# Kernel tuning notes

Hardware: AMD Instinct MI355X
Metric: run time of the kernel (lower is better)

The kernel has to match this reference:

```python
import jax, jax.numpy as jnp
import numpy as np

U_DECAY = 0.97
X_DECAY = 0.97
LN_EPS = 1e-5   # torch F.layer_norm default
L1_EPS = 1e-12  # torch F.normalize default


def _ln(x):
    # layer_norm over last dim, no affine params
    m = jnp.mean(x, axis=-1, keepdims=True)
    v = jnp.mean((x - m) ** 2, axis=-1, keepdims=True)
    return (x - m) * jax.lax.rsqrt(v + LN_EPS)


def setup_inputs() -> dict:
    key = jax.random.key(0)
    k0, k1, k2, k3 = jax.random.split(key, 4)
    B, T, d, n = 8, 256, 256, 1024
    embeddings = jax.random.normal(k0, (B, T, d), dtype=jnp.float32)
    E = jax.random.normal(k1, (d, n), dtype=jnp.float32) / n ** 0.5
    Dx = jax.random.normal(k2, (n, d), dtype=jnp.float32) / d ** 0.5
    Dy = jax.random.normal(k3, (n, d), dtype=jnp.float32) / d ** 0.5
    return {"embeddings": embeddings, "E": E, "Dx": Dx, "Dy": Dy}


def reference(embeddings, E, Dx, Dy):
    B, T, d = embeddings.shape
    n = E.shape[1]

    def step(carry, v_prev):  # v_prev: (B, d)
        x_state, rho = carry  # (B, n), (B, d, n)
        x_update = jax.nn.relu(v_prev @ Dx.T)                      # (B, n)
        x_t = X_DECAY * x_state + x_update
        x_t = x_t / jnp.maximum(jnp.sum(jnp.abs(x_t), axis=-1, keepdims=True), L1_EPS)  # L1 normalize
        a_star = jnp.einsum('bdn,bn->bd', rho, x_t)                # (B, d)
        y_core = _ln(a_star) @ Dy.T                                # (B, n)
        y_t = jax.nn.relu(y_core) * jax.nn.relu(x_t)               # (B, n)
        v_star = _ln(y_t @ E.T)                                    # (B, d)
        rho_t = U_DECAY * rho + _ln(v_prev)[:, :, None] * x_t[:, None, :]  # (B, d, n)
        return (x_t, rho_t), v_star

    x0 = jnp.zeros((B, n), dtype=embeddings.dtype)
    rho0 = jnp.zeros((B, d, n), dtype=embeddings.dtype)
    _, vs = jax.lax.scan(step, (x0, rho0), jnp.swapaxes(embeddings, 0, 1))  # vs: (T, B, d)
    return jnp.swapaxes(vs, 0, 1)  # (B, T, d)
```

## Files before the change

### kernel.cpp

```cpp
#include <hip/hip_runtime.h>
#include <math.h>


#define TT 256
#define BB 8
#define DD 256
#define NN 1024
#define ROWS (BB*TT)

using f16   = _Float16;
using f16x4 = __attribute__((ext_vector_type(4))) _Float16;
using f16x8 = __attribute__((ext_vector_type(8))) _Float16;
using f32x4 = __attribute__((ext_vector_type(4))) float;

__device__ inline f32x4 mfma16(f16x8 a, f16x8 b, f32x4 c) {
    return __builtin_amdgcn_mfma_f32_16x16x32_f16(a, b, c, 0, 0, 0);
}

__launch_bounds__(256)
__global__ void cvtln_kernel(const float* __restrict__ emb, const float* __restrict__ E,
                             const float* __restrict__ Dx, const float* __restrict__ Dy,
                             f16* __restrict__ embf, f16* __restrict__ Ef,
                             f16* __restrict__ Dxf, f16* __restrict__ Dyf,
                             f16* __restrict__ lnvTf) {
    __shared__ f16 sT[256][24];
    if (blockIdx.x < 1280) {
        int base = (blockIdx.x * 256 + threadIdx.x) * 4;
        const float* s; f16* d; int loc;
        if      (base <  524288) { s = emb; d = embf; loc = base; }
        else if (base <  786432) { s = E;   d = Ef;   loc = base - 524288; }
        else if (base < 1048576) { s = Dx;  d = Dxf;  loc = base - 786432; }
        else                     { s = Dy;  d = Dyf;  loc = base - 1048576; }
        float4 v = *(const float4*)(s + loc);
        f16x4 h = {(f16)v.x, (f16)v.y, (f16)v.z, (f16)v.w};
        *(f16x4*)(d + loc) = h;
        return;
    }
    const int bx = blockIdx.x - 1280;
    const int b  = bx >> 4;
    const int t0 = (bx & 15) * 16;
    const int wave = threadIdx.x >> 6;
    const int lane = threadIdx.x & 63;
#pragma unroll
    for (int rr = 0; rr < 4; ++rr) {
        int tloc = wave * 4 + rr;
        const float* p = emb + ((size_t)b * TT + t0 + tloc) * DD;
        float4 v = *(const float4*)(p + lane * 4);
        float s  = v.x + v.y + v.z + v.w;
        float s2 = v.x*v.x + v.y*v.y + v.z*v.z + v.w*v.w;
#pragma unroll
        for (int o = 32; o; o >>= 1) {
            s  += __shfl_xor(s,  o, 64);
            s2 += __shfl_xor(s2, o, 64);
        }
        float m   = s * (1.0f / 256.0f);
        float sc  = rsqrtf(s2 * (1.0f / 256.0f) - m * m + 1e-5f);
        sT[lane * 4 + 0][tloc] = (f16)((v.x - m) * sc);
        sT[lane * 4 + 1][tloc] = (f16)((v.y - m) * sc);
        sT[lane * 4 + 2][tloc] = (f16)((v.z - m) * sc);
        sT[lane * 4 + 3][tloc] = (f16)((v.w - m) * sc);
    }
    __syncthreads();
    int j = threadIdx.x;
    size_t o = ((size_t)b * DD + j) * TT + t0;
    *(f16x8*)(lnvTf + o)     = *(const f16x8*)&sT[j][0];
    *(f16x8*)(lnvTf + o + 8) = *(const f16x8*)&sT[j][8];
}

__launch_bounds__(256)
__global__ void k_xu(const f16* __restrict__ A, const f16* __restrict__ B,
                     f16* __restrict__ xuh, float* __restrict__ Spart) {
    const int i0 = blockIdx.y * 64, j0 = blockIdx.x * 128;
    const int t = threadIdx.x, lane = t & 63, wid = t >> 6;
    const int wr = wid >> 1, wc = wid & 1;
    const int lr = lane >> 4, lc = lane & 15;
    __shared__ __align__(16) f16 sA[2][64][40], sB[2][128][40];
    __shared__ float ssum[64][2];
    const int arow = t >> 2, akq = (t & 3) * 8;
    f32x4 acc[2][4];
    const f32x4 z4 = {0.f, 0.f, 0.f, 0.f};
#pragma unroll
    for (int fi = 0; fi < 2; ++fi)
#pragma unroll
        for (int fj = 0; fj < 4; ++fj) acc[fi][fj] = z4;

    const int NT = DD / 32;
    const f16* pa  = A + (size_t)(i0 + arow) * DD + akq;
    const f16* pb0 = B + (size_t)(j0 + arow) * DD + akq;
    const f16* pb1 = B + (size_t)(j0 + 64 + arow) * DD + akq;
    f16x8 va  = *(const f16x8*)pa;
    f16x8 vb0 = *(const f16x8*)pb0;
    f16x8 vb1 = *(const f16x8*)pb1;
    *(f16x8*)&sA[0][arow][akq]      = va;
    *(f16x8*)&sB[0][arow][akq]      = vb0;
    *(f16x8*)&sB[0][64 + arow][akq] = vb1;
    __syncthreads();
    int cur = 0;
    for (int kt = 0; kt < NT; ++kt) {
        if (kt + 1 < NT) {
            int ko = (kt + 1) * 32;
            va  = *(const f16x8*)(pa + ko);
            vb0 = *(const f16x8*)(pb0 + ko);
            vb1 = *(const f16x8*)(pb1 + ko);
        }
        f16x8 ah[2], bh[4];
#pragma unroll
        for (int fi = 0; fi < 2; ++fi)
            ah[fi] = *(const f16x8*)&sA[cur][wr * 32 + fi * 16 + lc][lr * 8];
#pragma unroll
        for (int fj = 0; fj < 4; ++fj)
            bh[fj] = *(const f16x8*)&sB[cur][wc * 64 + fj * 16 + lc][lr * 8];
#pragma unroll
        for (int fi = 0; fi < 2; ++fi)
#pragma unroll
            for (int fj = 0; fj < 4; ++fj)
                acc[fi][fj] = mfma16(ah[fi], bh[fj], acc[fi][fj]);
        if (kt + 1 < NT) {
            *(f16x8*)&sA[cur ^ 1][arow][akq]      = va;
            *(f16x8*)&sB[cur ^ 1][arow][akq]      = vb0;
            *(f16x8*)&sB[cur ^ 1][64 + arow][akq] = vb1;
            __syncthreads();
            cur ^= 1;
        }
    }
    float rs[2][4] = {};
#pragma unroll
    for (int fi = 0; fi < 2; ++fi)
#pragma unroll
        for (int fj = 0; fj < 4; ++fj) {
            f32x4 d = acc[fi][fj];
#pragma unroll
            for (int r = 0; r < 4; ++r) {
                int i = i0 + wr * 32 + fi * 16 + lr * 4 + r;
                int j = j0 + wc * 64 + fj * 16 + lc;
                float vv = fmaxf(d[r], 0.f);
                xuh[(size_t)i * NN + j] = (f16)vv;
                rs[fi][r] += vv;
            }
        }
#pragma unroll
    for (int fi = 0; fi < 2; ++fi)
#pragma unroll
        for (int r = 0; r < 4; ++r) {
            float v = rs[fi][r];
#pragma unroll
            for (int m = 1; m < 16; m <<= 1) v += __shfl_xor(v, m, 64);
            if (lc == 0) ssum[wr * 32 + fi * 16 + lr * 4 + r][wc] = v;
        }
    __syncthreads();
    if (t < 64) Spart[(size_t)blockIdx.x * ROWS + i0 + t] = ssum[t][0] + ssum[t][1];
}

__launch_bounds__(256)
__global__ void k_xscan(const f16* __restrict__ xuh, const float* __restrict__ Spart,
                        f16* __restrict__ xf) {
    __shared__ float Gs[16][16], Hs[16][16], Cs[16][16];
    __shared__ float sS[256], sRC[256];
    __shared__ int bad;
    const int b = blockIdx.x >> 6, jgrp = blockIdx.x & 63;
    const int tid = threadIdx.x;
    float s = 0.f;
#pragma unroll
    for (int g = 0; g < 8; ++g) s += Spart[(size_t)g * ROWS + b * TT + tid];
    if (tid == 0) bad = 0;
    sS[tid] = s;
    __syncthreads();
    float us = (tid == 0) ? s : (0.97f + s);
    if (us < 1e-12f) bad = 1;
    __syncthreads();
    if (!bad) {
        sRC[tid] = 1.0f / us;
    } else if (tid == 0) {
        float sigma = 0.f;
        for (int tt = 0; tt < TT; ++tt) {
            float u2 = fmaf(0.97f, sigma, sS[tt]);
            float r  = 1.0f / fmaxf(u2, 1e-12f);
            sRC[tt] = r;
            sigma = u2 * r;
        }
    }
    __syncthreads();

    const int ck = tid >> 4, jl = tid & 15;
    const int j  = jgrp * 16 + jl;
    const size_t base = ((size_t)b * TT + ck * 16) * NN + j;
    float xur[16], rcr[16];
#pragma unroll
    for (int i = 0; i < 16; ++i) xur[i] = (float)xuh[base + (size_t)i * NN];
#pragma unroll
    for (int i = 0; i < 16; ++i) rcr[i] = sRC[ck * 16 + i];
    float xs = 0.f, G = 1.f;
#pragma unroll
    for (int i = 0; i < 16; ++i) {
        xs = fmaf(0.97f, xs, xur[i]) * rcr[i];
        G *= 0.97f * rcr[i];
    }
    Gs[ck][jl] = G;
    Hs[ck][jl] = xs;
    __syncthreads();
    if (tid < 16) {
        float cr = 0.f;
        Cs[0][tid] = 0.f;
#pragma unroll
        for (int cc = 0; cc < 15; ++cc) {
            cr = fmaf(Gs[cc][tid], cr, Hs[cc][tid]);
            Cs[cc + 1][tid] = cr;
        }
    }
    __syncthreads();
    xs = Cs[ck][jl];
#pragma unroll
    for (int i = 0; i < 16; ++i) {
        xs = fmaf(0.97f, xs, xur[i]) * rcr[i];
        xf[base + (size_t)i * NN] = (f16)xs;
    }
}

template <int EPI>
__launch_bounds__(256)
__global__ void g64_kernel(const f16* __restrict__ A, const f16* __restrict__ B,
                           float* __restrict__ Cf, f16* __restrict__ Ch,
                           int N, int ld, int Kloop,
                           long long sA_, long long sB_, long long sC_) {
    const int z = blockIdx.z;
    A += (size_t)z * sA_; B += (size_t)z * sB_;
    if (EPI == 0) Cf += (size_t)z * sC_; else Ch += (size_t)z * sC_;
    const int i0 = blockIdx.y * 64, j0 = blockIdx.x * 64;
    const int t = threadIdx.x, lane = t & 63, wid = t >> 6;
    const int wr = wid >> 1, wc = wid & 1;
    const int lr = lane >> 4, lc = lane & 15;
    const float L2D = -0.043943348f;

    if (EPI == 3 && j0 > i0) {
#pragma unroll
        for (int fi = 0; fi < 2; ++fi)
#pragma unroll
            for (int fj = 0; fj < 2; ++fj)
#pragma unroll
                for (int r = 0; r < 4; ++r) {
                    int i = i0 + wr * 32 + fi * 16 + lr * 4 + r;
                    int j = j0 + wc * 32 + fj * 16 + lc;
                    Ch[(size_t)i * N + j] = (f16)0.f;
                }
        return;
    }

    __shared__ __align__(16) f16 sA[2][64][40], sB[2][64][40];
    const int srow = t >> 2, skq = (t & 3) * 8;
    f32x4 acc[2][2];
    const f32x4 z4 = {0.f, 0.f, 0.f, 0.f};
    acc[0][0] = z4; acc[0][1] = z4; acc[1][0] = z4; acc[1][1] = z4;

    const int NT = Kloop / 32;
    const f16* pa = A + (size_t)(i0 + srow) * ld + skq;
    const f16* pb = B + (size_t)(j0 + srow) * ld + skq;
    f16x8 va = *(const f16x8*)pa;
    f16x8 vb = *(const f16x8*)pb;
    *(f16x8*)&sA[0][srow][skq] = va;
    *(f16x8*)&sB[0][srow][skq] = vb;
    __syncthreads();
    int cur = 0;
    for (int kt = 0; kt < NT; ++kt) {
        if (kt + 1 < NT) {
            va = *(const f16x8*)(pa + (kt + 1) * 32);
            vb = *(const f16x8*)(pb + (kt + 1) * 32);
        }
        f16x8 ah0 = *(const f16x8*)&sA[cur][wr * 32 + lc][lr * 8];
        f16x8 ah1 = *(const f16x8*)&sA[cur][wr * 32 + 16 + lc][lr * 8];
        f16x8 bh0 = *(const f16x8*)&sB[cur][wc * 32 + lc][lr * 8];
        f16x8 bh1 = *(const f16x8*)&sB[cur][wc * 32 + 16 + lc][lr * 8];
        acc[0][0] = mfma16(ah0, bh0, acc[0][0]);
        acc[0][1] = mfma16(ah0, bh1, acc[0][1]);
        acc[1][0] = mfma16(ah1, bh0, acc[1][0]);
        acc[1][1] = mfma16(ah1, bh1, acc[1][1]);
        if (kt + 1 < NT) {
            *(f16x8*)&sA[cur ^ 1][srow][skq] = va;
            *(f16x8*)&sB[cur ^ 1][srow][skq] = vb;
            __syncthreads();
            cur ^= 1;
        }
    }
#pragma unroll
    for (int fi = 0; fi < 2; ++fi)
#pragma unroll
        for (int fj = 0; fj < 2; ++fj) {
            f32x4 d = acc[fi][fj];
#pragma unroll
            for (int r = 0; r < 4; ++r) {
                int i = i0 + wr * 32 + fi * 16 + lr * 4 + r;
                int j = j0 + wc * 32 + fj * 16 + lc;
                size_t o = (size_t)i * N + j;
                if (EPI == 0) {
                    Cf[o] = d[r];
                } else {
                    float w = 0.f;
                    if (j < i) w = exp2f((float)(i - 1 - j) * L2D) * d[r];
                    Ch[o] = (f16)w;
                }
            }
        }
}

__launch_bounds__(256)
__global__ void k_aln(const f16* __restrict__ Wf, const f16* __restrict__ lnvTf,
                      f16* __restrict__ alnf) {
    const int b = blockIdx.y;
    const int i0 = blockIdx.x * 16;
    const f16* A = Wf + (size_t)b * TT * TT;
    const f16* B = lnvTf + (size_t)b * DD * TT;
    const int t = threadIdx.x, lane = t & 63, w = t >> 6;
    const int lr = lane >> 4, lc = lane & 15;
    __shared__ __align__(16) f16 sA[2][16][40], sB[2][256][40];
    __shared__ float sS[4][16], sS2[4][16];
    const int arow = t >> 2, akq = (t & 3) * 8;
    const int brow = t >> 2, bkq = (t & 3) * 8;
    f32x4 acc[4];
    const f32x4 z4 = {0.f, 0.f, 0.f, 0.f};
#pragma unroll
    for (int f = 0; f < 4; ++f) acc[f] = z4;

    const int NT = TT / 32;
    const f16* pa = A + (size_t)(i0 + arow) * TT + akq;
    const f16* pb = B + (size_t)brow * TT + bkq;
    f16x8 va;
    f16x8 vb[4];
    if (t < 64) va = *(const f16x8*)pa;
#pragma unroll
    for (int q = 0; q < 4; ++q)
        vb[q] = *(const f16x8*)(pb + (size_t)q * 64 * TT);
    if (t < 64) *(f16x8*)&sA[0][arow][akq] = va;
#pragma unroll
    for (int q = 0; q < 4; ++q)
        *(f16x8*)&sB[0][q * 64 + brow][bkq] = vb[q];
    __syncthreads();
    int cur = 0;
    for (int kt = 0; kt < NT; ++kt) {
        if (kt + 1 < NT) {
            int ko = (kt + 1) * 32;
            if (t < 64) va = *(const f16x8*)(pa + ko);
#pragma unroll
            for (int q = 0; q < 4; ++q)
                vb[q] = *(const f16x8*)(pb + (size_t)q * 64 * TT + ko);
        }
        f16x8 af = *(const f16x8*)&sA[cur][lc][lr * 8];
#pragma unroll
        for (int f = 0; f < 4; ++f) {
            f16x8 bf = *(const f16x8*)&sB[cur][w * 64 + f * 16 + lc][lr * 8];
            acc[f] = mfma16(af, bf, acc[f]);
        }
        if (kt + 1 < NT) {
            if (t < 64) *(f16x8*)&sA[cur ^ 1][arow][akq] = va;
#pragma unroll
            for (int q = 0; q < 4; ++q)
                *(f16x8*)&sB[cur ^ 1][q * 64 + brow][bkq] = vb[q];
            __syncthreads();
            cur ^= 1;
        }
    }
    float s[4] = {}, s2[4] = {};
#pragma unroll
    for (int f = 0; f < 4; ++f)
#pragma unroll
        for (int r = 0; r < 4; ++r) { float v = acc[f][r]; s[r] += v; s2[r] += v * v; }
#pragma unroll
    for (int m = 1; m < 16; m <<= 1)
#pragma unroll
        for (int r = 0; r < 4; ++r) {
            s[r]  += __shfl_xor(s[r],  m, 64);
            s2[r] += __shfl_xor(s2[r], m, 64);
        }
    if (lc == 0)
#pragma unroll
        for (int r = 0; r < 4; ++r) { sS[w][lr * 4 + r] = s[r]; sS2[w][lr * 4 + r] = s2[r]; }
    __syncthreads();
    float mean[4], rstd[4];
#pragma unroll
    for (int r = 0; r < 4; ++r) {
        int row = lr * 4 + r;
        float tot  = sS[0][row] + sS[1][row] + sS[2][row] + sS[3][row];
        float tot2 = sS2[0][row] + sS2[1][row] + sS2[2][row] + sS2[3][row];
        mean[r] = tot * (1.f / 256.f);
        rstd[r] = rsqrtf(tot2 * (1.f / 256.f) - mean[r] * mean[r] + 1e-5f);
    }
#pragma unroll
    for (int f = 0; f < 4; ++f)
#pragma unroll
        for (int r = 0; r < 4; ++r) {
            int i = i0 + lr * 4 + r;
            int j = w * 64 + f * 16 + lc;
            alnf[((size_t)b * TT + i) * DD + j] = (f16)((acc[f][r] - mean[r]) * rstd[r]);
        }
}

__launch_bounds__(256)
__global__ void k_y(const f16* __restrict__ A, const f16* __restrict__ B,
                    f16* __restrict__ yf, const f16* __restrict__ xf) {
    const int i0 = blockIdx.y * 64, j0 = blockIdx.x * 128;
    const int t = threadIdx.x, lane = t & 63, wid = t >> 6;
    const int wr = wid >> 1, wc = wid & 1;
    const int lr = lane >> 4, lc = lane & 15;
    __shared__ __align__(16) f16 sA[2][64][40], sB[2][128][40];
    const int arow = t >> 2, akq = (t & 3) * 8;
    f32x4 acc[2][4];
    const f32x4 z4 = {0.f, 0.f, 0.f, 0.f};
#pragma unroll
    for (int fi = 0; fi < 2; ++fi)
#pragma unroll
        for (int fj = 0; fj < 4; ++fj) acc[fi][fj] = z4;

    const int NT = DD / 32;
    const f16* pa  = A + (size_t)(i0 + arow) * DD + akq;
    const f16* pb0 = B + (size_t)(j0 + arow) * DD + akq;
    const f16* pb1 = B + (size_t)(j0 + 64 + arow) * DD + akq;
    f16x8 va  = *(const f16x8*)pa;
    f16x8 vb0 = *(const f16x8*)pb0;
    f16x8 vb1 = *(const f16x8*)pb1;
    *(f16x8*)&sA[0][arow][akq]      = va;
    *(f16x8*)&sB[0][arow][akq]      = vb0;
    *(f16x8*)&sB[0][64 + arow][akq] = vb1;
    __syncthreads();
    int cur = 0;
    for (int kt = 0; kt < NT; ++kt) {
        if (kt + 1 < NT) {
            int ko = (kt + 1) * 32;
            va  = *(const f16x8*)(pa + ko);
            vb0 = *(const f16x8*)(pb0 + ko);
            vb1 = *(const f16x8*)(pb1 + ko);
        }
        f16x8 ah[2], bh[4];
#pragma unroll
        for (int fi = 0; fi < 2; ++fi)
            ah[fi] = *(const f16x8*)&sA[cur][wr * 32 + fi * 16 + lc][lr * 8];
#pragma unroll
        for (int fj = 0; fj < 4; ++fj)
            bh[fj] = *(const f16x8*)&sB[cur][wc * 64 + fj * 16 + lc][lr * 8];
#pragma unroll
        for (int fi = 0; fi < 2; ++fi)
#pragma unroll
            for (int fj = 0; fj < 4; ++fj)
                acc[fi][fj] = mfma16(ah[fi], bh[fj], acc[fi][fj]);
        if (kt + 1 < NT) {
            *(f16x8*)&sA[cur ^ 1][arow][akq]      = va;
            *(f16x8*)&sB[cur ^ 1][arow][akq]      = vb0;
            *(f16x8*)&sB[cur ^ 1][64 + arow][akq] = vb1;
            __syncthreads();
            cur ^= 1;
        }
    }
#pragma unroll
    for (int fi = 0; fi < 2; ++fi)
#pragma unroll
        for (int fj = 0; fj < 4; ++fj) {
            f32x4 d = acc[fi][fj];
#pragma unroll
            for (int r = 0; r < 4; ++r) {
                int i = i0 + wr * 32 + fi * 16 + lr * 4 + r;
                int j = j0 + wc * 64 + fj * 16 + lc;
                size_t o = (size_t)i * NN + j;
                float vv = fmaxf(d[r], 0.f) * (float)xf[o];
                yf[o] = (f16)vv;
            }
        }
}

__launch_bounds__(256)
__global__ void ln2_kernel(const float* __restrict__ in, const float* __restrict__ in2,
                           float* __restrict__ outf) {
    int wave = threadIdx.x >> 6;
    int lane = threadIdx.x & 63;
    int row  = blockIdx.x * 4 + wave;
    float4 v = *(const float4*)(in + (size_t)row * DD + lane * 4);
    float4 w = *(const float4*)(in2 + (size_t)row * DD + lane * 4);
    v.x += w.x; v.y += w.y; v.z += w.z; v.w += w.w;
    float s  = v.x + v.y + v.z + v.w;
    float s2 = v.x*v.x + v.y*v.y + v.z*v.z + v.w*v.w;
#pragma unroll
    for (int o = 32; o; o >>= 1) {
        s  += __shfl_xor(s,  o, 64);
        s2 += __shfl_xor(s2, o, 64);
    }
    float m  = s * (1.0f / 256.0f);
    float sc = rsqrtf(s2 * (1.0f / 256.0f) - m * m + 1e-5f);
    float4 o4 = {(v.x - m) * sc, (v.y - m) * sc, (v.z - m) * sc, (v.w - m) * sc};
    *(float4*)(outf + (size_t)row * DD + lane * 4) = o4;
}

extern "C" void kernel_launch(void* const* d_in, const int* in_sizes, int n_in,
                              void* d_out, int out_size, void* d_ws, size_t ws_size,
                              hipStream_t stream) {
    (void)in_sizes; (void)n_in; (void)out_size; (void)ws_size;
    const float* emb = (const float*)d_in[0];
    const float* E   = (const float*)d_in[1];
    const float* Dx  = (const float*)d_in[2];
    const float* Dy  = (const float*)d_in[3];
    float* out = (float*)d_out;

    char* wsb = (char*)d_ws;
    f16*   embf  = (f16*)(wsb + 0);
    f16*   Ef    = (f16*)(wsb + 1048576);
    f16*   Dxf   = (f16*)(wsb + 1572864);
    f16*   Dyf   = (f16*)(wsb + 2097152);
    f16*   lnvTf = (f16*)(wsb + 2621440);
    f16*   xuh   = (f16*)(wsb + 3670016);
    f16*   xf    = (f16*)(wsb + 7864320);
    f16*   Wf    = (f16*)(wsb + 12058624);
    f16*   alnf  = (f16*)(wsb + 13107200);
    f16*   yf    = (f16*)(wsb + 14155776);
    float* vpart = (float*)(wsb + 18350080);
    float* Spart = (float*)(wsb + 22544384);

    cvtln_kernel<<<1280 + ROWS / 16, 256, 0, stream>>>(
        emb, E, Dx, Dy, embf, Ef, Dxf, Dyf, lnvTf);
    k_xu<<<dim3(NN / 128, ROWS / 64), 256, 0, stream>>>(embf, Dxf, xuh, Spart);
    k_xscan<<<BB * (NN / 16), 256, 0, stream>>>(xuh, Spart, xf);
    g64_kernel<3><<<dim3(TT / 64, TT / 64, BB), 256, 0, stream>>>(
        xf, xf, nullptr, Wf, TT, NN, NN,
        (long long)TT * NN, (long long)TT * NN, (long long)TT * TT);
    k_aln<<<dim3(TT / 16, BB), 256, 0, stream>>>(Wf, lnvTf, alnf);
    k_y<<<dim3(NN / 128, ROWS / 64), 256, 0, stream>>>(alnf, Dyf, yf, xf);
    g64_kernel<0><<<dim3(DD / 64, ROWS / 64, 2), 256, 0, stream>>>(
        yf, Ef, vpart, nullptr, DD, NN, 512,
        512LL, 512LL, (long long)ROWS * DD);
    ln2_kernel<<<ROWS / 4, 256, 0, stream>>>(
        vpart, vpart + (size_t)ROWS * DD, out);
}
```

Baseline: 60.67 us.

## Fuse final LayerNorm into split-K GEMM via atomic counter; widen xscan chunks

Removes the separate ln2 launch. The split-K v GEMM's blocks now increment a per-row-tile atomic counter, and the last of the 8 blocks per row tile sums both K halves and applies LayerNorm, writing the output directly. The counter is zeroed in the first kernel. Separately, the x scan now uses 32-step chunks over 32 columns per block, which halves the block count and shortens the serial carry across chunks, at the cost of more registers per thread. The generic GEMM template is also specialised into a dedicated W kernel.

```diff
diff --git a/kernel.cpp b/kernel.cpp
--- a/kernel.cpp
+++ b/kernel.cpp
@@ -22,8 +22,9 @@
                              const float* __restrict__ Dx, const float* __restrict__ Dy,
                              f16* __restrict__ embf, f16* __restrict__ Ef,
                              f16* __restrict__ Dxf, f16* __restrict__ Dyf,
-                             f16* __restrict__ lnvTf) {
+                             f16* __restrict__ lnvTf, int* __restrict__ cnt) {
     __shared__ f16 sT[256][24];
+    if (blockIdx.x == 0 && threadIdx.x < 32) cnt[threadIdx.x] = 0;
     if (blockIdx.x < 1280) {
         int base = (blockIdx.x * 256 + threadIdx.x) * 4;
         const float* s; f16* d; int loc;
@@ -154,10 +155,10 @@
 __launch_bounds__(256)
 __global__ void k_xscan(const f16* __restrict__ xuh, const float* __restrict__ Spart,
                         f16* __restrict__ xf) {
-    __shared__ float Gs[16][16], Hs[16][16], Cs[16][16];
+    __shared__ float Gs[8][33], Hs[8][33], Cs[8][33];
     __shared__ float sS[256], sRC[256];
     __shared__ int bad;
-    const int b = blockIdx.x >> 6, jgrp = blockIdx.x & 63;
+    const int b = blockIdx.x >> 5, jgrp = blockIdx.x & 31;
     const int tid = threadIdx.x;
     float s = 0.f;
 #pragma unroll
@@ -181,28 +182,28 @@
     }
     __syncthreads();
 
-    const int ck = tid >> 4, jl = tid & 15;
-    const int j  = jgrp * 16 + jl;
-    const size_t base = ((size_t)b * TT + ck * 16) * NN + j;
-    float xur[16], rcr[16];
-#pragma unroll
-    for (int i = 0; i < 16; ++i) xur[i] = (float)xuh[base + (size_t)i * NN];
-#pragma unroll
-    for (int i = 0; i < 16; ++i) rcr[i] = sRC[ck * 16 + i];
+    const int ck = tid >> 5, jl = tid & 31;
+    const int j  = jgrp * 32 + jl;
+    const size_t base = ((size_t)b * TT + ck * 32) * NN + j;
+    float xur[32], rcr[32];
+#pragma unroll
+    for (int i = 0; i < 32; ++i) xur[i] = (float)xuh[base + (size_t)i * NN];
+#pragma unroll
+    for (int i = 0; i < 32; ++i) rcr[i] = sRC[ck * 32 + i];
     float xs = 0.f, G = 1.f;
 #pragma unroll
-    for (int i = 0; i < 16; ++i) {
+    for (int i = 0; i < 32; ++i) {
         xs = fmaf(0.97f, xs, xur[i]) * rcr[i];
         G *= 0.97f * rcr[i];
     }
     Gs[ck][jl] = G;
     Hs[ck][jl] = xs;
     __syncthreads();
-    if (tid < 16) {
+    if (tid < 32) {
         float cr = 0.f;
         Cs[0][tid] = 0.f;
 #pragma unroll
-        for (int cc = 0; cc < 15; ++cc) {
+        for (int cc = 0; cc < 7; ++cc) {
             cr = fmaf(Gs[cc][tid], cr, Hs[cc][tid]);
             Cs[cc + 1][tid] = cr;
         }
@@ -210,28 +211,24 @@
     __syncthreads();
     xs = Cs[ck][jl];
 #pragma unroll
-    for (int i = 0; i < 16; ++i) {
+    for (int i = 0; i < 32; ++i) {
         xs = fmaf(0.97f, xs, xur[i]) * rcr[i];
         xf[base + (size_t)i * NN] = (f16)xs;
     }
 }
 
-template <int EPI>
-__launch_bounds__(256)
-__global__ void g64_kernel(const f16* __restrict__ A, const f16* __restrict__ B,
-                           float* __restrict__ Cf, f16* __restrict__ Ch,
-                           int N, int ld, int Kloop,
-                           long long sA_, long long sB_, long long sC_) {
-    const int z = blockIdx.z;
-    A += (size_t)z * sA_; B += (size_t)z * sB_;
-    if (EPI == 0) Cf += (size_t)z * sC_; else Ch += (size_t)z * sC_;
+__launch_bounds__(256)
+__global__ void k_W(const f16* __restrict__ xf, f16* __restrict__ Wf) {
+    const int b = blockIdx.z;
+    const f16* X = xf + (size_t)b * TT * NN;
+    f16* Wb = Wf + (size_t)b * TT * TT;
     const int i0 = blockIdx.y * 64, j0 = blockIdx.x * 64;
     const int t = threadIdx.x, lane = t & 63, wid = t >> 6;
     const int wr = wid >> 1, wc = wid & 1;
     const int lr = lane >> 4, lc = lane & 15;
     const float L2D = -0.043943348f;
 
-    if (EPI == 3 && j0 > i0) {
+    if (j0 > i0) {
 #pragma unroll
         for (int fi = 0; fi < 2; ++fi)
 #pragma unroll
@@ -240,7 +237,7 @@
                 for (int r = 0; r < 4; ++r) {
                     int i = i0 + wr * 32 + fi * 16 + lr * 4 + r;
                     int j = j0 + wc * 32 + fj * 16 + lc;
-                    Ch[(size_t)i * N + j] = (f16)0.f;
+                    Wb[(size_t)i * TT + j] = (f16)0.f;
                 }
         return;
     }
@@ -251,9 +248,9 @@
     const f32x4 z4 = {0.f, 0.f, 0.f, 0.f};
     acc[0][0] = z4; acc[0][1] = z4; acc[1][0] = z4; acc[1][1] = z4;
 
-    const int NT = Kloop / 32;
-    const f16* pa = A + (size_t)(i0 + srow) * ld + skq;
-    const f16* pb = B + (size_t)(j0 + srow) * ld + skq;
+    const int NT = NN / 32;
+    const f16* pa = X + (size_t)(i0 + srow) * NN + skq;
+    const f16* pb = X + (size_t)(j0 + srow) * NN + skq;
     f16x8 va = *(const f16x8*)pa;
     f16x8 vb = *(const f16x8*)pb;
     *(f16x8*)&sA[0][srow][skq] = va;
@@ -289,14 +286,9 @@
             for (int r = 0; r < 4; ++r) {
                 int i = i0 + wr * 32 + fi * 16 + lr * 4 + r;
                 int j = j0 + wc * 32 + fj * 16 + lc;
-                size_t o = (size_t)i * N + j;
-                if (EPI == 0) {
-                    Cf[o] = d[r];
-                } else {
-                    float w = 0.f;
-                    if (j < i) w = exp2f((float)(i - 1 - j) * L2D) * d[r];
-                    Ch[o] = (f16)w;
-                }
+                float w = 0.f;
+                if (j < i) w = exp2f((float)(i - 1 - j) * L2D) * d[r];
+                Wb[(size_t)i * TT + j] = (f16)w;
             }
         }
 }
@@ -313,7 +305,6 @@
     __shared__ __align__(16) f16 sA[2][16][40], sB[2][256][40];
     __shared__ float sS[4][16], sS2[4][16];
     const int arow = t >> 2, akq = (t & 3) * 8;
-    const int brow = t >> 2, bkq = (t & 3) * 8;
     f32x4 acc[4];
     const f32x4 z4 = {0.f, 0.f, 0.f, 0.f};
 #pragma unroll
@@ -321,7 +312,7 @@
 
     const int NT = TT / 32;
     const f16* pa = A + (size_t)(i0 + arow) * TT + akq;
-    const f16* pb = B + (size_t)brow * TT + bkq;
+    const f16* pb = B + (size_t)arow * TT + akq;
     f16x8 va;
     f16x8 vb[4];
     if (t < 64) va = *(const f16x8*)pa;
@@ -331,7 +322,7 @@
     if (t < 64) *(f16x8*)&sA[0][arow][akq] = va;
 #pragma unroll
     for (int q = 0; q < 4; ++q)
-        *(f16x8*)&sB[0][q * 64 + brow][bkq] = vb[q];
+        *(f16x8*)&sB[0][q * 64 + arow][akq] = vb[q];
     __syncthreads();
     int cur = 0;
     for (int kt = 0; kt < NT; ++kt) {
@@ -352,7 +343,7 @@
             if (t < 64) *(f16x8*)&sA[cur ^ 1][arow][akq] = va;
 #pragma unroll
             for (int q = 0; q < 4; ++q)
-                *(f16x8*)&sB[cur ^ 1][q * 64 + brow][bkq] = vb[q];
+                *(f16x8*)&sB[cur ^ 1][q * 64 + arow][akq] = vb[q];
             __syncthreads();
             cur ^= 1;
         }
@@ -464,25 +455,90 @@
 }
 
 __launch_bounds__(256)
-__global__ void ln2_kernel(const float* __restrict__ in, const float* __restrict__ in2,
-                           float* __restrict__ outf) {
-    int wave = threadIdx.x >> 6;
-    int lane = threadIdx.x & 63;
-    int row  = blockIdx.x * 4 + wave;
-    float4 v = *(const float4*)(in + (size_t)row * DD + lane * 4);
-    float4 w = *(const float4*)(in2 + (size_t)row * DD + lane * 4);
-    v.x += w.x; v.y += w.y; v.z += w.z; v.w += w.w;
-    float s  = v.x + v.y + v.z + v.w;
-    float s2 = v.x*v.x + v.y*v.y + v.z*v.z + v.w*v.w;
-#pragma unroll
-    for (int o = 32; o; o >>= 1) {
-        s  += __shfl_xor(s,  o, 64);
-        s2 += __shfl_xor(s2, o, 64);
-    }
-    float m  = s * (1.0f / 256.0f);
-    float sc = rsqrtf(s2 * (1.0f / 256.0f) - m * m + 1e-5f);
-    float4 o4 = {(v.x - m) * sc, (v.y - m) * sc, (v.z - m) * sc, (v.w - m) * sc};
-    *(float4*)(outf + (size_t)row * DD + lane * 4) = o4;
+__global__ void k_vg(const f16* __restrict__ yf, const f16* __restrict__ Ef,
+                     float* __restrict__ vpart, int* __restrict__ cnt,
+                     float* __restrict__ out) {
+    const int z = blockIdx.z;
+    float* C = vpart + (size_t)z * ROWS * DD;
+    const int i0 = blockIdx.y * 64, j0 = blockIdx.x * 64;
+    const int t = threadIdx.x, lane = t & 63, wid = t >> 6;
+    const int wr = wid >> 1, wc = wid & 1;
+    const int lr = lane >> 4, lc = lane & 15;
+    __shared__ __align__(16) f16 sA[2][64][40], sB[2][64][40];
+    __shared__ int lastFlag;
+    const int srow = t >> 2, skq = (t & 3) * 8;
+    f32x4 acc[2][2];
+    const f32x4 z4 = {0.f, 0.f, 0.f, 0.f};
+    acc[0][0] = z4; acc[0][1] = z4; acc[1][0] = z4; acc[1][1] = z4;
+
+    const int NT = 512 / 32;
+    const f16* pa = yf + (size_t)(i0 + srow) * NN + z * 512 + skq;
+    const f16* pb = Ef + (size_t)(j0 + srow) * NN + z * 512 + skq;
+    f16x8 va = *(const f16x8*)pa;
+    f16x8 vb = *(const f16x8*)pb;
+    *(f16x8*)&sA[0][srow][skq] = va;
+    *(f16x8*)&sB[0][srow][skq] = vb;
+    __syncthreads();
+    int cur = 0;
+    for (int kt = 0; kt < NT; ++kt) {
+        if (kt + 1 < NT) {
+            va = *(const f16x8*)(pa + (kt + 1) * 32);
+            vb = *(const f16x8*)(pb + (kt + 1) * 32);
+        }
+        f16x8 ah0 = *(const f16x8*)&sA[cur][wr * 32 + lc][lr * 8];
+        f16x8 ah1 = *(const f16x8*)&sA[cur][wr * 32 + 16 + lc][lr * 8];
+        f16x8 bh0 = *(const f16x8*)&sB[cur][wc * 32 + lc][lr * 8];
+        f16x8 bh1 = *(const f16x8*)&sB[cur][wc * 32 + 16 + lc][lr * 8];
+        acc[0][0] = mfma16(ah0, bh0, acc[0][0]);
+        acc[0][1] = mfma16(ah0, bh1, acc[0][1]);
+        acc[1][0] = mfma16(ah1, bh0, acc[1][0]);
+        acc[1][1] = mfma16(ah1, bh1, acc[1][1]);
+        if (kt + 1 < NT) {
+            *(f16x8*)&sA[cur ^ 1][srow][skq] = va;
+            *(f16x8*)&sB[cur ^ 1][srow][skq] = vb;
+            __syncthreads();
+            cur ^= 1;
+        }
+    }
+#pragma unroll
+    for (int fi = 0; fi < 2; ++fi)
+#pragma unroll
+        for (int fj = 0; fj < 2; ++fj) {
+            f32x4 d = acc[fi][fj];
+#pragma unroll
+            for (int r = 0; r < 4; ++r) {
+                int i = i0 + wr * 32 + fi * 16 + lr * 4 + r;
+                int j = j0 + wc * 32 + fj * 16 + lc;
+                C[(size_t)i * DD + j] = d[r];
+            }
+        }
+
+    __threadfence();
+    if (t == 0) {
+        int old = atomicAdd(&cnt[blockIdx.y], 1);
+        lastFlag = (old == 7);
+    }
+    __syncthreads();
+    if (!lastFlag) return;
+    __threadfence();
+#pragma unroll
+    for (int u = 0; u < 16; ++u) {
+        int row = i0 + u * 4 + wid;
+        float4 v = *(const float4*)(vpart + (size_t)row * DD + lane * 4);
+        float4 w = *(const float4*)(vpart + (size_t)(ROWS + row) * DD + lane * 4);
+        v.x += w.x; v.y += w.y; v.z += w.z; v.w += w.w;
+        float s  = v.x + v.y + v.z + v.w;
+        float s2 = v.x*v.x + v.y*v.y + v.z*v.z + v.w*v.w;
+#pragma unroll
+        for (int o = 32; o; o >>= 1) {
+            s  += __shfl_xor(s,  o, 64);
+            s2 += __shfl_xor(s2, o, 64);
+        }
+        float m  = s * (1.0f / 256.0f);
+        float sc = rsqrtf(s2 * (1.0f / 256.0f) - m * m + 1e-5f);
+        float4 o4 = {(v.x - m) * sc, (v.y - m) * sc, (v.z - m) * sc, (v.w - m) * sc};
+        *(float4*)(out + (size_t)row * DD + lane * 4) = o4;
+    }
 }
 
 extern "C" void kernel_launch(void* const* d_in, const int* in_sizes, int n_in,
@@ -508,19 +564,14 @@
     f16*   yf    = (f16*)(wsb + 14155776);
     float* vpart = (float*)(wsb + 18350080);
     float* Spart = (float*)(wsb + 22544384);
+    int*   cnt   = (int*)(wsb + 22609920);
 
     cvtln_kernel<<<1280 + ROWS / 16, 256, 0, stream>>>(
-        emb, E, Dx, Dy, embf, Ef, Dxf, Dyf, lnvTf);
+        emb, E, Dx, Dy, embf, Ef, Dxf, Dyf, lnvTf, cnt);
     k_xu<<<dim3(NN / 128, ROWS / 64), 256, 0, stream>>>(embf, Dxf, xuh, Spart);
-    k_xscan<<<BB * (NN / 16), 256, 0, stream>>>(xuh, Spart, xf);
-    g64_kernel<3><<<dim3(TT / 64, TT / 64, BB), 256, 0, stream>>>(
-        xf, xf, nullptr, Wf, TT, NN, NN,
-        (long long)TT * NN, (long long)TT * NN, (long long)TT * TT);
+    k_xscan<<<BB * 32, 256, 0, stream>>>(xuh, Spart, xf);
+    k_W<<<dim3(TT / 64, TT / 64, BB), 256, 0, stream>>>(xf, Wf);
     k_aln<<<dim3(TT / 16, BB), 256, 0, stream>>>(Wf, lnvTf, alnf);
     k_y<<<dim3(NN / 128, ROWS / 64), 256, 0, stream>>>(alnf, Dyf, yf, xf);
-    g64_kernel<0><<<dim3(DD / 64, ROWS / 64, 2), 256, 0, stream>>>(
-        yf, Ef, vpart, nullptr, DD, NN, 512,
-        512LL, 512LL, (long long)ROWS * DD);
-    ln2_kernel<<<ROWS / 4, 256, 0, stream>>>(
-        vpart, vpart + (size_t)ROWS * DD, out);
-}
+    k_vg<<<dim3(DD / 64, ROWS / 64, 2), 256, 0, stream>>>(yf, Ef, vpart, cnt, out);
+}
```

Measured after the change: 88.66 us. 1.46x slower.
